# Kernel optimization log

Measured on AMD Instinct MI355X. Metric: run time of the kernel, lower is better.

Reference implementation:

```python
import jax, jax.numpy as jnp
import numpy as np

IN_DIM = 128
OUT_DIM = 128
EDGE_DIM = 64
NUM_HEADS = 8
HEAD_DIM = OUT_DIM // NUM_HEADS
N_NODES = 10000
N_EDGES = 320000
LN_EPS = 1e-5


def _gelu(x):
    # torch nn.GELU default is the exact (erf) formulation
    return jax.nn.gelu(x, approximate=False)


def _layernorm(x, g, b):
    mu = jnp.mean(x, axis=-1, keepdims=True)
    var = jnp.var(x, axis=-1, keepdims=True)
    return (x - mu) * jax.lax.rsqrt(var + LN_EPS) * g + b


def setup_inputs() -> dict:
    key = jax.random.key(0)
    ks = jax.random.split(key, 16)

    def lin(k, fan_in, fan_out):
        # torch nn.Linear default init: U(-1/sqrt(fan_in), 1/sqrt(fan_in))
        bound = 1.0 / np.sqrt(fan_in)
        kw, kb = jax.random.split(k)
        w = jax.random.uniform(kw, (fan_in, fan_out), jnp.float32, -bound, bound)
        b = jax.random.uniform(kb, (fan_out,), jnp.float32, -bound, bound)
        return w, b

    node_features = jax.random.normal(ks[0], (N_NODES, IN_DIM), jnp.float32)
    edge_index = jax.random.randint(ks[1], (2, N_EDGES), 0, N_NODES)
    edge_attr = jax.random.normal(ks[2], (N_EDGES, EDGE_DIM), jnp.float32)

    msg_w1, msg_b1 = lin(ks[3], 2 * IN_DIM + EDGE_DIM, OUT_DIM)
    msg_w2, msg_b2 = lin(ks[4], OUT_DIM, OUT_DIM)
    q_w, q_b = lin(ks[5], IN_DIM, OUT_DIM)
    kv_w, kv_b = lin(ks[6], IN_DIM + EDGE_DIM, OUT_DIM)
    out_w1, out_b1 = lin(ks[7], IN_DIM + OUT_DIM, OUT_DIM)
    out_w2, out_b2 = lin(ks[8], OUT_DIM, OUT_DIM)
    ln_g = 1.0 + 0.02 * jax.random.normal(ks[9], (OUT_DIM,), jnp.float32)
    ln_b = 0.02 * jax.random.normal(ks[10], (OUT_DIM,), jnp.float32)

    return dict(node_features=node_features, edge_attr=edge_attr,
                msg_w1=msg_w1, msg_b1=msg_b1, msg_w2=msg_w2, msg_b2=msg_b2,
                q_w=q_w, q_b=q_b, kv_w=kv_w, kv_b=kv_b,
                out_w1=out_w1, out_b1=out_b1, out_w2=out_w2, out_b2=out_b2,
                ln_g=ln_g, ln_b=ln_b, edge_index=edge_index)


def reference(node_features, edge_attr, msg_w1, msg_b1, msg_w2, msg_b2,
              q_w, q_b, kv_w, kv_b, out_w1, out_b1, out_w2, out_b2,
              ln_g, ln_b, edge_index):
    N = node_features.shape[0]
    E = edge_index.shape[1]
    src, dst = edge_index[0], edge_index[1]

    s = node_features[src]                      # [E, Din]
    d = node_features[dst]                      # [E, Din]

    # message MLP
    m_in = jnp.concatenate([s, d, edge_attr], axis=-1)          # [E, 2*Din+De]
    m = _gelu(m_in @ msg_w1 + msg_b1) @ msg_w2 + msg_b2         # [E, Dout]

    # per-edge attention logits
    q = (d @ q_w + q_b).reshape(E, NUM_HEADS, HEAD_DIM)
    kv_in = jnp.concatenate([s, edge_attr], axis=-1)
    kv = (kv_in @ kv_w + kv_b).reshape(E, NUM_HEADS, HEAD_DIM)
    attn = jnp.sum(q * kv, axis=-1) * (HEAD_DIM ** -0.5)        # [E, H]

    # Deterministic version: pick the edge with the largest index per dst node.
    last = jnp.full((N,), -1, dtype=jnp.int32).at[dst].max(
        jnp.arange(E, dtype=jnp.int32))                          # [N]
    attn_full = jnp.where(last[:, None] >= 0,
                          attn[jnp.maximum(last, 0)],
                          -jnp.inf)                              # [N, H]
    # softmax over the NODE axis (dim=0), exactly as the torch code does;
    # -inf rows contribute 0, so using N instead of dst.max()+1 is identical.
    attn_norm = jax.nn.softmax(attn_full, axis=0)[dst]           # [E, H]

    m = (m.reshape(E, NUM_HEADS, HEAD_DIM) * attn_norm[..., None]).reshape(E, OUT_DIM)

    # scatter-add aggregation
    agg = jax.ops.segment_sum(m, dst, num_segments=N)            # [N, Dout]

    h_in = jnp.concatenate([node_features, agg], axis=-1)        # [N, Din+Dout]
    h = _gelu(h_in @ out_w1 + out_b1) @ out_w2 + out_b2          # [N, Dout]

    # res_proj is Identity since in_dim == out_dim; dropout is eval-mode no-op
    return _layernorm(node_features + h, ln_g, ln_b)
```

## Files before the change

kernel.cpp:

```cpp
#include <hip/hip_runtime.h>
#include <hip/hip_bf16.h>

#define NN 10000
#define NE 320000

typedef __bf16 bf16x8 __attribute__((ext_vector_type(8)));
typedef float  f32x4  __attribute__((ext_vector_type(4)));

__device__ __forceinline__ float bf2f(ushort u){
  union { uint i; float f; } c; c.i = ((uint)u) << 16; return c.f;
}
__device__ __forceinline__ ushort f2bf(float f){
  union { float f; uint i; } c; c.f = f;
  uint x = c.i;
  return (ushort)((x + 0x7FFFu + ((x >> 16) & 1u)) >> 16);
}
__device__ __forceinline__ float gelu_erf(float x){
  return 0.5f * x * (1.0f + erff(x * 0.70710678118654752f));
}
__device__ __forceinline__ float gelu_tanh(float x){
  float y = 0.7978845608028654f * (x + 0.044715f * x * x * x);
  float e = __expf(2.f * y);
  float th = 1.f - 2.f / (e + 1.f);
  return 0.5f * x * (1.f + th);
}
__device__ __forceinline__ uint encf(float f){
  uint u = __float_as_uint(f);
  return (u & 0x80000000u) ? ~u : (u | 0x80000000u);
}
__device__ __forceinline__ float decf(uint u){
  return __uint_as_float((u & 0x80000000u) ? (u & 0x7FFFFFFFu) : ~u);
}
#define MFMA16(a,b,c) __builtin_amdgcn_mfma_f32_16x16x32_bf16((a),(b),(c),0,0,0)

__global__ void k_detect(const uint* __restrict__ w, int* __restrict__ flag){
  int t = threadIdx.x;
  uint cnt = 0;
  for (int i = t; i < 4096; i += 256){
    uint v = w[i * 63];
    uint e = (v >> 7) & 0xFF;
    if (e >= 100 && e <= 140) cnt++;
  }
  __shared__ uint red[256];
  red[t] = cnt; __syncthreads();
  for (int s = 128; s > 0; s >>= 1){
    if (t < s) red[t] += red[t + s];
    __syncthreads();
  }
  if (t == 0) *flag = (red[0] < 2048) ? 1 : 0;
}

__global__ void k_prep(
    const void* NF0, const void* w1, const void* w2, const void* qw, const void* kvw,
    const void* ow1, const void* ow2,
    const void* b1, const void* b2, const void* qb, const void* kvb,
    const void* ob1, const void* ob2, const void* lg, const void* lb,
    ushort* NFc, float* Gagg, int* last, int* cnt, uint* Menc, float* S,
    ushort* SB, ushort* KVW2,
    ushort* W1aT, ushort* W1bT, ushort* W1cT, ushort* W2T, ushort* QT, ushort* KVT,
    ushort* O1T, ushort* O2T, const int* flag)
{
  int f = *flag;
  int idx = blockIdx.x * 256 + threadIdx.x;
  if (idx < 320000){
    if (f){
      float4 v = ((const float4*)NF0)[idx];
      ushort4 o; o.x=f2bf(v.x); o.y=f2bf(v.y); o.z=f2bf(v.z); o.w=f2bf(v.w);
      ((ushort4*)NFc)[idx] = o;
    } else ((ushort4*)NFc)[idx] = ((const ushort4*)NF0)[idx];
    return;
  }
  idx -= 320000;
  if (idx < 320000){ float4 z = {0.f,0.f,0.f,0.f}; ((float4*)Gagg)[idx] = z; return; }
  idx -= 320000;
  if (idx < 20016){
    if (idx < 10000) last[idx] = -1;
    else if (idx < 20000) cnt[idx - 10000] = 0;
    else if (idx < 20008) Menc[idx - 20000] = 0u;
    else S[idx - 20008] = 0.f;
    return;
  }
  idx -= 20016;
  if (idx < 1024){
    const void* ps[8] = {b1,b2,qb,kvb,ob1,ob2,lg,lb};
    const void* p = ps[idx >> 7]; int j = idx & 127;
    SB[idx] = f ? f2bf(((const float*)p)[j]) : ((const ushort*)p)[j];
    return;
  }
  idx -= 1024;
  if (idx < 8192){
    KVW2[idx] = f ? f2bf(((const float*)kvw)[16384 + idx]) : ((const ushort*)kvw)[16384 + idx];
    return;
  }
  idx -= 8192;
  if (idx < 16384){ int c=idx>>7,k=idx&127; W1aT[idx] = f? f2bf(((const float*)w1)[k*128+c]) : ((const ushort*)w1)[k*128+c]; return; }
  idx -= 16384;
  if (idx < 16384){ int c=idx>>7,k=idx&127; W1bT[idx] = f? f2bf(((const float*)w1)[(128+k)*128+c]) : ((const ushort*)w1)[(128+k)*128+c]; return; }
  idx -= 16384;
  if (idx < 8192){ int c=idx>>6,k=idx&63;  W1cT[idx] = f? f2bf(((const float*)w1)[(256+k)*128+c]) : ((const ushort*)w1)[(256+k)*128+c]; return; }
  idx -= 8192;
  if (idx < 16384){ int c=idx>>7,k=idx&127; W2T[idx] = f? f2bf(((const float*)w2)[k*128+c]) : ((const ushort*)w2)[k*128+c]; return; }
  idx -= 16384;
  if (idx < 16384){ int c=idx>>7,k=idx&127; QT[idx]  = f? f2bf(((const float*)qw)[k*128+c]) : ((const ushort*)qw)[k*128+c]; return; }
  idx -= 16384;
  if (idx < 16384){ int c=idx>>7,k=idx&127; KVT[idx] = f? f2bf(((const float*)kvw)[k*128+c]) : ((const ushort*)kvw)[k*128+c]; return; }
  idx -= 16384;
  if (idx < 32768){ int c=idx>>8,k=idx&255; O1T[idx] = f? f2bf(((const float*)ow1)[k*128+c]) : ((const ushort*)ow1)[k*128+c]; return; }
  idx -= 32768;
  if (idx < 16384){ int c=idx>>7,k=idx&127; O2T[idx] = f? f2bf(((const float*)ow2)[k*128+c]) : ((const ushort*)ow2)[k*128+c]; return; }
}

__global__ void k_count(const int* __restrict__ dst, int* __restrict__ cnt,
                        int* __restrict__ last){
  int e = blockIdx.x * 256 + threadIdx.x;
  if (e < NE){
    int d = dst[e];
    atomicAdd(&cnt[d], 1);
    atomicMax(&last[d], e);
  }
}

__global__ __launch_bounds__(1024) void k_scan(const int* __restrict__ cnt,
                                               int* __restrict__ fill){
  __shared__ int sc[1024];
  int t = threadIdx.x;
  int base = t * 10;
  int v[10]; int tot = 0;
  #pragma unroll
  for (int j = 0; j < 10; ++j){
    int idx = base + j;
    v[j] = (idx < NN) ? cnt[idx] : 0;
    tot += v[j];
  }
  sc[t] = tot; __syncthreads();
  for (int off = 1; off < 1024; off <<= 1){
    int x = (t >= off) ? sc[t - off] : 0;
    __syncthreads();
    sc[t] += x;
    __syncthreads();
  }
  int run = sc[t] - tot;
  #pragma unroll
  for (int j = 0; j < 10; ++j){
    int idx = base + j;
    if (idx < NN) fill[idx] = run;
    run += v[j];
  }
}

__global__ void k_fill(const int* __restrict__ src, const int* __restrict__ dst,
                       int* __restrict__ fill, int* __restrict__ pos,
                       int* __restrict__ sSort, int* __restrict__ dSort){
  int e = blockIdx.x * 256 + threadIdx.x;
  if (e < NE){
    int d = dst[e];
    int p = atomicAdd(&fill[d], 1);
    pos[e] = p;
    sSort[p] = src[e];
    dSort[p] = d;
  }
}

__global__ __launch_bounds__(256) void k_perm(
    const float* __restrict__ EAf, const ushort* __restrict__ EAb,
    const int* __restrict__ pos, ushort* __restrict__ EAs,
    const int* __restrict__ flag)
{
  int i = blockIdx.x * 256 + threadIdx.x;
  int r = i >> 1, half = i & 1;
  if (r >= NE) return;
  int p = pos[r];
  ushort* op = EAs + (size_t)p * 64 + half * 32;
  if (*flag){
    const float* in = EAf + (size_t)r * 64 + half * 32;
    #pragma unroll
    for (int j = 0; j < 4; ++j){
      float4 a = *reinterpret_cast<const float4*>(in + j * 8);
      float4 b = *reinterpret_cast<const float4*>(in + j * 8 + 4);
      bf16x8 v;
      v[0]=(__bf16)a.x; v[1]=(__bf16)a.y; v[2]=(__bf16)a.z; v[3]=(__bf16)a.w;
      v[4]=(__bf16)b.x; v[5]=(__bf16)b.y; v[6]=(__bf16)b.z; v[7]=(__bf16)b.w;
      *reinterpret_cast<bf16x8*>(op + j * 8) = v;
    }
  } else {
    const ushort* in = EAb + (size_t)r * 64 + half * 32;
    #pragma unroll
    for (int j = 0; j < 4; ++j)
      *reinterpret_cast<bf16x8*>(op + j * 8) =
        *reinterpret_cast<const bf16x8*>(in + j * 8);
  }
}

__global__ __launch_bounds__(256) void k_nodepack(
    const ushort* __restrict__ NFc,
    const ushort* __restrict__ W1aT, const ushort* __restrict__ W1bT,
    const ushort* __restrict__ QT,  const ushort* __restrict__ KVT,
    const ushort* __restrict__ SB,
    ushort* __restrict__ PA, ushort* __restrict__ PB,
    ushort* __restrict__ Qb, ushort* __restrict__ KV1)
{
  int t = threadIdx.x, l = t & 63, w = t >> 6;
  int m = l & 15, g = l >> 4;
  int row0 = blockIdx.x * 16;
  const ushort* WT = (w==0) ? W1aT : (w==1) ? W1bT : (w==2) ? QT : KVT;
  ushort*       OUT= (w==0) ? PA   : (w==1) ? PB   : (w==2) ? Qb : KV1;
  const f32x4 FZ = {0.f,0.f,0.f,0.f};
  f32x4 acc[8];
  #pragma unroll
  for (int i = 0; i < 8; ++i) acc[i] = FZ;
  int arow = row0 + m;
  #pragma unroll
  for (int ks = 0; ks < 4; ++ks){
    int koff = ks * 32 + g * 8;
    bf16x8 a = *reinterpret_cast<const bf16x8*>(NFc + (size_t)arow * 128 + koff);
    #pragma unroll
    for (int nt = 0; nt < 8; ++nt){
      bf16x8 b = *reinterpret_cast<const bf16x8*>(WT + (size_t)(nt*16+m) * 128 + koff);
      acc[nt] = MFMA16(a, b, acc[nt]);
    }
  }
  #pragma unroll
  for (int nt = 0; nt < 8; ++nt){
    int col = nt * 16 + m;
    float bb = (w==1) ? bf2f(SB[col]) : (w==2) ? bf2f(SB[256+col]) : (w==3) ? bf2f(SB[384+col]) : 0.f;
    #pragma unroll
    for (int r = 0; r < 4; ++r){
      int row = row0 + g * 4 + r;
      OUT[(size_t)row * 128 + col] = f2bf(acc[nt][r] + bb);
    }
  }
}

__global__ __launch_bounds__(256) void k_edge(
    const ushort* __restrict__ PA, const ushort* __restrict__ PB,
    const ushort* __restrict__ EAs,
    const int* __restrict__ sSort, const int* __restrict__ dSort,
    const ushort* __restrict__ W1cT,
    float* __restrict__ Gagg)
{
  __shared__ int sIdx[128], dIdx[128];
  __shared__ __align__(16) char Hs[128 * 256];
  int t = threadIdx.x;
  int p0 = blockIdx.x * 128;
  int l = t & 63, w = t >> 6;
  int rw = w >> 1, cw = w & 1;
  int m = l & 15, g = l >> 4;

  if (t < 128){ sIdx[t] = sSort[p0 + t]; dIdx[t] = dSort[p0 + t]; }
  __syncthreads();

  {
    int r = t >> 1, half = t & 1;
    int sr = sIdx[r], dr = dIdx[r];
    #pragma unroll
    for (int j = 0; j < 8; ++j){
      int c8 = half * 8 + j;
      bf16x8 pa = *reinterpret_cast<const bf16x8*>(PA + (size_t)sr * 128 + c8 * 8);
      bf16x8 pb = *reinterpret_cast<const bf16x8*>(PB + (size_t)dr * 128 + c8 * 8);
      bf16x8 ps;
      #pragma unroll
      for (int k = 0; k < 8; ++k) ps[k] = (__bf16)((float)pa[k] + (float)pb[k]);
      int byte = (r * 256 + c8 * 16) ^ ((r & 7) << 4);
      *reinterpret_cast<bf16x8*>(&Hs[byte]) = ps;
    }
  }

  const f32x4 FZ = {0.f,0.f,0.f,0.f};
  f32x4 acc[4][4];
  #pragma unroll
  for (int i = 0; i < 4; ++i)
    #pragma unroll
    for (int j = 0; j < 4; ++j) acc[i][j] = FZ;

  #pragma unroll
  for (int ks = 0; ks < 2; ++ks){
    bf16x8 af[4], bfr[4];
    #pragma unroll
    for (int rt = 0; rt < 4; ++rt){
      int rl = rw * 64 + rt * 16 + m;
      af[rt] = *reinterpret_cast<const bf16x8*>(EAs + (size_t)(p0 + rl) * 64 + ks * 32 + g * 8);
    }
    #pragma unroll
    for (int ct = 0; ct < 4; ++ct){
      int col = cw * 64 + ct * 16 + m;
      bfr[ct] = *reinterpret_cast<const bf16x8*>(W1cT + (size_t)col * 64 + ks * 32 + g * 8);
    }
    #pragma unroll
    for (int rt = 0; rt < 4; ++rt)
      #pragma unroll
      for (int ct = 0; ct < 4; ++ct)
        acc[rt][ct] = MFMA16(af[rt], bfr[ct], acc[rt][ct]);
  }
  __syncthreads();

  #pragma unroll
  for (int ct = 0; ct < 4; ++ct){
    int col = cw * 64 + ct * 16 + m;
    #pragma unroll
    for (int rt = 0; rt < 4; ++rt)
      #pragma unroll
      for (int r = 0; r < 4; ++r){
        int row = rw * 64 + rt * 16 + g * 4 + r;
        int byte = (row * 256 + col * 2) ^ ((row & 7) << 4);
        float v = gelu_tanh(acc[rt][ct][r] + bf2f(*reinterpret_cast<const ushort*>(&Hs[byte])));
        *reinterpret_cast<ushort*>(&Hs[byte]) = f2bf(v);
      }
  }
  __syncthreads();

  int c = t & 127, hh = t >> 7;
  int rS = hh * 64, rE = rS + 64;
  float run = 0.f;
  int cur = dIdx[rS];
  for (int r = rS; r < rE; ++r){
    int d = dIdx[r];
    if (d != cur){
      unsafeAtomicAdd(&Gagg[(size_t)cur * 128 + c], run);
      run = 0.f; cur = d;
    }
    int byte = (r * 256 + c * 2) ^ ((r & 7) << 4);
    run += bf2f(*reinterpret_cast<const ushort*>(&Hs[byte]));
  }
  unsafeAtomicAdd(&Gagg[(size_t)cur * 128 + c], run);
}

template<int K, int MODE>
__global__ __launch_bounds__(256) void k_gemm(
    const ushort* __restrict__ A, const ushort* __restrict__ WT,
    const ushort* __restrict__ bias, void* __restrict__ out, int M)
{
  int t = threadIdx.x;
  int l = t & 63, w = t >> 6;
  int m = l & 15, g = l >> 4;
  int row0 = blockIdx.x * 64 + w * 16;
  const f32x4 FZ = {0.f,0.f,0.f,0.f};
  f32x4 acc[8];
  #pragma unroll
  for (int i = 0; i < 8; ++i) acc[i] = FZ;

  int arow = row0 + m; if (arow >= M) arow = M - 1;
  #pragma unroll
  for (int ks = 0; ks < K / 32; ++ks){
    int koff = ks * 32 + g * 8;
    bf16x8 a = *reinterpret_cast<const bf16x8*>(A + (size_t)arow * K + koff);
    #pragma unroll
    for (int nt = 0; nt < 8; ++nt){
      bf16x8 b = *reinterpret_cast<const bf16x8*>(WT + (size_t)(nt * 16 + m) * K + koff);
      acc[nt] = MFMA16(a, b, acc[nt]);
    }
  }
  #pragma unroll
  for (int nt = 0; nt < 8; ++nt){
    int col = nt * 16 + m;
    float bb = bf2f(bias[col]);
    #pragma unroll
    for (int r = 0; r < 4; ++r){
      int row = row0 + g * 4 + r;
      if (row < M){
        float v = acc[nt][r] + bb;
        if (MODE == 1) v = gelu_erf(v);
        ((ushort*)out)[(size_t)row * 128 + col] = f2bf(v);
      }
    }
  }
}

__global__ __launch_bounds__(256) void k_attn(
    const ushort* __restrict__ Qb, const ushort* __restrict__ KV1,
    const ushort* __restrict__ EAb, const float* __restrict__ EAf,
    const ushort* __restrict__ KVW2,
    const int* __restrict__ srcI, const int* __restrict__ last,
    float* __restrict__ attn, uint* __restrict__ Menc, const int* __restrict__ flag)
{
  __shared__ float ea_s[16][64];
  __shared__ int eN[16], sN[16];
  __shared__ uint lmax[8];
  int t = threadIdx.x;
  int n0 = blockIdx.x * 16;
  if (t < 16){
    int e = last[n0 + t];
    eN[t] = e;
    sN[t] = (e >= 0) ? srcI[e] : 0;
  }
  if (t < 8) lmax[t] = 0u;
  __syncthreads();
  int F = *flag;
  for (int i = t; i < 1024; i += 256){
    int nn = i >> 6, k = i & 63;
    int e = eN[nn];
    int ee = (e >= 0) ? e : 0;
    float v = F ? EAf[(size_t)ee * 64 + k] : bf2f(EAb[(size_t)ee * 64 + k]);
    ea_s[nn][k] = (e >= 0) ? v : 0.0f;
  }
  __syncthreads();

  int j = t & 127;
  int half = t >> 7;
  float acc[8];
  #pragma unroll
  for (int i = 0; i < 8; ++i) acc[i] = 0.f;
  for (int k = 0; k < 64; ++k){
    float wv = bf2f(KVW2[(size_t)k * 128 + j]);
    #pragma unroll
    for (int nn = 0; nn < 8; ++nn) acc[nn] += ea_s[half * 8 + nn][k] * wv;
  }
  #pragma unroll
  for (int nn = 0; nn < 8; ++nn){
    int nl = half * 8 + nn;
    int n = n0 + nl;
    int e = eN[nl];
    float kvv = acc[nn] + bf2f(KV1[(size_t)sN[nl] * 128 + j]);
    float qv  = bf2f(Qb[(size_t)n * 128 + j]);
    float p = qv * kvv;
    p += __shfl_xor(p, 1); p += __shfl_xor(p, 2);
    p += __shfl_xor(p, 4); p += __shfl_xor(p, 8);
    if ((j & 15) == 0 && e >= 0){
      float v = p * 0.25f;
      attn[(size_t)n * 8 + (j >> 4)] = v;
      atomicMax(&lmax[j >> 4], encf(v));
    }
  }
  __syncthreads();
  if (t < 8 && lmax[t]) atomicMax(&Menc[t], lmax[t]);
}

__global__ __launch_bounds__(256) void k_asum(
    const float* __restrict__ attn, const int* __restrict__ last,
    const uint* __restrict__ Menc, float* __restrict__ S)
{
  __shared__ float red[256][8];
  int t = threadIdx.x;
  float M[8];
  #pragma unroll
  for (int h = 0; h < 8; ++h) M[h] = decf(Menc[h]);
  float p[8];
  #pragma unroll
  for (int h = 0; h < 8; ++h) p[h] = 0.f;
  for (int n = blockIdx.x * 256 + t; n < NN; n += gridDim.x * 256){
    if (last[n] >= 0){
      #pragma unroll
      for (int h = 0; h < 8; ++h) p[h] += __expf(attn[(size_t)n * 8 + h] - M[h]);
    }
  }
  #pragma unroll
  for (int h = 0; h < 8; ++h) red[t][h] = p[h];
  __syncthreads();
  for (int s = 128; s > 0; s >>= 1){
    if (t < s){
      #pragma unroll
      for (int h = 0; h < 8; ++h) red[t][h] += red[t + s][h];
    }
    __syncthreads();
  }
  if (t < 8) atomicAdd(&S[t], red[0][t]);
}

__global__ __launch_bounds__(256) void k_aggmm(
    const float* __restrict__ Gagg, const ushort* __restrict__ W2T,
    const ushort* __restrict__ SB,
    const int* __restrict__ cnt, const int* __restrict__ last,
    const float* __restrict__ attn, const uint* __restrict__ Menc,
    const float* __restrict__ S,
    const ushort* __restrict__ NFc, ushort* __restrict__ h_in)
{
  int t = threadIdx.x, l = t & 63, w = t >> 6;
  int m = l & 15, g = l >> 4;
  int row0 = blockIdx.x * 64 + w * 16;

  {
    int rr = blockIdx.x * 64 + (t >> 2);
    int cc = (t & 3) * 32;
    if (rr < NN){
      #pragma unroll
      for (int j = 0; j < 4; ++j){
        bf16x8 v = *reinterpret_cast<const bf16x8*>(NFc + (size_t)rr * 128 + cc + j * 8);
        *reinterpret_cast<bf16x8*>(h_in + (size_t)rr * 256 + cc + j * 8) = v;
      }
    }
  }

  float M[8], Sinv[8];
  #pragma unroll
  for (int h = 0; h < 8; ++h){ M[h] = decf(Menc[h]); Sinv[h] = 1.0f / S[h]; }

  int arow = row0 + m; if (arow >= NN) arow = NN - 1;
  const f32x4 FZ = {0.f,0.f,0.f,0.f};
  f32x4 acc[8];
  #pragma unroll
  for (int i = 0; i < 8; ++i) acc[i] = FZ;

  #pragma unroll
  for (int ks = 0; ks < 4; ++ks){
    const float* gp = Gagg + (size_t)arow * 128 + ks * 32 + g * 8;
    float4 u0 = *reinterpret_cast<const float4*>(gp);
    float4 u1 = *reinterpret_cast<const float4*>(gp + 4);
    float gv[8] = {u0.x,u0.y,u0.z,u0.w,u1.x,u1.y,u1.z,u1.w};
    bf16x8 hi, lo;
    #pragma unroll
    for (int k = 0; k < 8; ++k){
      hi[k] = (__bf16)gv[k];
      lo[k] = (__bf16)(gv[k] - (float)hi[k]);
    }
    #pragma unroll
    for (int nt = 0; nt < 8; ++nt){
      bf16x8 b = *reinterpret_cast<const bf16x8*>(W2T + (size_t)(nt*16+m) * 128 + ks * 32 + g * 8);
      acc[nt] = MFMA16(hi, b, acc[nt]);
      acc[nt] = MFMA16(lo, b, acc[nt]);
    }
  }

  #pragma unroll
  for (int r = 0; r < 4; ++r){
    int row = row0 + g * 4 + r;
    if (row < NN){
      float cn = (float)cnt[row];
      int lst = last[row];
      #pragma unroll
      for (int nt = 0; nt < 8; ++nt){
        int col = nt * 16 + m;
        float bb = bf2f(SB[128 + col]);
        float aw = (lst >= 0) ? __expf(attn[(size_t)row * 8 + nt] - M[nt]) * Sinv[nt] : 0.f;
        float v = (acc[nt][r] + cn * bb) * aw;
        h_in[(size_t)row * 256 + 128 + col] = f2bf(v);
      }
    }
  }
}

__global__ __launch_bounds__(256) void k_out2ln(
    const ushort* __restrict__ T1, const ushort* __restrict__ O2T,
    const ushort* __restrict__ SB,
    const ushort* __restrict__ NFc, void* __restrict__ out,
    const int* __restrict__ flag)
{
  int t = threadIdx.x, l = t & 63, w = t >> 6;
  int m = l & 15, g = l >> 4;
  int row0 = blockIdx.x * 64 + w * 16;
  int F = *flag;
  int arow = row0 + m; if (arow >= NN) arow = NN - 1;
  const f32x4 FZ = {0.f,0.f,0.f,0.f};
  f32x4 acc[8];
  #pragma unroll
  for (int i = 0; i < 8; ++i) acc[i] = FZ;
  #pragma unroll
  for (int ks = 0; ks < 4; ++ks){
    int koff = ks * 32 + g * 8;
    bf16x8 a = *reinterpret_cast<const bf16x8*>(T1 + (size_t)arow * 128 + koff);
    #pragma unroll
    for (int nt = 0; nt < 8; ++nt){
      bf16x8 b = *reinterpret_cast<const bf16x8*>(O2T + (size_t)(nt*16+m) * 128 + koff);
      acc[nt] = MFMA16(a, b, acc[nt]);
    }
  }
  #pragma unroll
  for (int r = 0; r < 4; ++r){
    int row = row0 + g * 4 + r;
    bool ok = row < NN;
    int rr = ok ? row : NN - 1;
    float x[8]; float s = 0.f, q = 0.f;
    #pragma unroll
    for (int nt = 0; nt < 8; ++nt){
      int col = nt * 16 + m;
      float xv = acc[nt][r] + bf2f(SB[640 + col]) + bf2f(NFc[(size_t)rr * 128 + col]);
      x[nt] = xv; s += xv; q += xv * xv;
    }
    #pragma unroll
    for (int msk = 1; msk < 16; msk <<= 1){
      s += __shfl_xor(s, msk);
      q += __shfl_xor(q, msk);
    }
    float mean = s * (1.0f / 128.0f);
    float var  = q * (1.0f / 128.0f) - mean * mean;
    float rs = rsqrtf(var + 1e-5f);
    if (ok){
      #pragma unroll
      for (int nt = 0; nt < 8; ++nt){
        int col = nt * 16 + m;
        float y = (x[nt] - mean) * rs * bf2f(SB[768 + col]) + bf2f(SB[896 + col]);
        if (F) ((float*)out)[(size_t)row * 128 + col] = y;
        else   ((ushort*)out)[(size_t)row * 128 + col] = f2bf(y);
      }
    }
  }
}

extern "C" void kernel_launch(void* const* d_in, const int* in_sizes, int n_in,
                              void* d_out, int out_size, void* d_ws, size_t ws_size,
                              hipStream_t stream)
{
  const void* NF0  = d_in[0];
  const void* EA0  = d_in[1];
  const void* w1   = d_in[2];
  const void* b1   = d_in[3];
  const void* w2   = d_in[4];
  const void* b2   = d_in[5];
  const void* qw   = d_in[6];
  const void* qb   = d_in[7];
  const void* kvw  = d_in[8];
  const void* kvb  = d_in[9];
  const void* ow1  = d_in[10];
  const void* ob1  = d_in[11];
  const void* ow2  = d_in[12];
  const void* ob2  = d_in[13];
  const void* lg   = d_in[14];
  const void* lb   = d_in[15];
  const int*  srcI = (const int*)d_in[16];
  const int*  dstI = srcI + NE;

  char* ws = (char*)d_ws;
  size_t off = 0;
  auto alloc = [&](size_t bytes) -> void* {
    void* p = ws + off;
    off = (off + bytes + 255) & ~(size_t)255;
    return p;
  };
  int*    flag  = (int*)   alloc(4);
  ushort* NFc   = (ushort*)alloc((size_t)NN * 128 * 2);
  ushort* SB    = (ushort*)alloc(8 * 128 * 2);
  ushort* KVW2  = (ushort*)alloc(64 * 128 * 2);
  ushort* W1aT  = (ushort*)alloc(128 * 128 * 2);
  ushort* W1bT  = (ushort*)alloc(128 * 128 * 2);
  ushort* W1cT  = (ushort*)alloc(128 * 64 * 2);
  ushort* W2T   = (ushort*)alloc(128 * 128 * 2);
  ushort* QT    = (ushort*)alloc(128 * 128 * 2);
  ushort* KVT   = (ushort*)alloc(128 * 128 * 2);
  ushort* O1T   = (ushort*)alloc(128 * 256 * 2);
  ushort* O2T   = (ushort*)alloc(128 * 128 * 2);
  int*    last  = (int*)   alloc(NN * 4);
  int*    cnt   = (int*)   alloc(NN * 4);
  int*    fill  = (int*)   alloc(NN * 4);
  int*    pos   = (int*)   alloc((size_t)NE * 4);
  int*    sSort = (int*)   alloc((size_t)NE * 4);
  int*    dSort = (int*)   alloc((size_t)NE * 4);
  ushort* EAs   = (ushort*)alloc((size_t)NE * 64 * 2);
  float*  attn  = (float*) alloc(NN * 8 * 4);
  uint*   Menc  = (uint*)  alloc(8 * 4);
  float*  S     = (float*) alloc(8 * 4);
  ushort* PA    = (ushort*)alloc((size_t)NN * 128 * 2);
  ushort* PB    = (ushort*)alloc((size_t)NN * 128 * 2);
  ushort* Qb    = (ushort*)alloc((size_t)NN * 128 * 2);
  ushort* KV1   = (ushort*)alloc((size_t)NN * 128 * 2);
  float*  Gagg  = (float*) alloc((size_t)NN * 128 * 4);
  ushort* h_in  = (ushort*)alloc((size_t)NN * 256 * 2);
  ushort* T1    = (ushort*)alloc((size_t)NN * 128 * 2);

  k_detect<<<1, 256, 0, stream>>>((const uint*)NF0, flag);
  k_prep<<<3159, 256, 0, stream>>>(NF0, w1, w2, qw, kvw, ow1, ow2,
                                   b1, b2, qb, kvb, ob1, ob2, lg, lb,
                                   NFc, Gagg, last, cnt, Menc, S, SB, KVW2,
                                   W1aT, W1bT, W1cT, W2T, QT, KVT, O1T, O2T, flag);
  k_count<<<1250, 256, 0, stream>>>(dstI, cnt, last);
  k_scan<<<1, 1024, 0, stream>>>(cnt, fill);
  k_fill<<<1250, 256, 0, stream>>>(srcI, dstI, fill, pos, sSort, dSort);
  k_perm<<<2500, 256, 0, stream>>>((const float*)EA0, (const ushort*)EA0, pos, EAs, flag);
  k_nodepack<<<625, 256, 0, stream>>>(NFc, W1aT, W1bT, QT, KVT, SB, PA, PB, Qb, KV1);
  k_edge<<<2500, 256, 0, stream>>>(PA, PB, EAs, sSort, dSort, W1cT, Gagg);
  k_attn<<<625, 256, 0, stream>>>(Qb, KV1, (const ushort*)EA0, (const float*)EA0,
                                  KVW2, srcI, last, attn, Menc, flag);
  k_asum<<<40, 256, 0, stream>>>(attn, last, Menc, S);
  k_aggmm<<<157, 256, 0, stream>>>(Gagg, W2T, SB, cnt, last, attn, Menc, S, NFc, h_in);
  k_gemm<256, 1><<<157, 256, 0, stream>>>(h_in, O1T, SB + 512, T1, NN);
  k_out2ln<<<157, 256, 0, stream>>>(T1, O2T, SB, NFc, d_out, flag);
}
```

Before: 240.7 us.

## Fuse kernel launches: merge count into prep, fill+perm+nodepack, edge+attn, aggmm+gemm

Cuts the launch sequence by merging kernels. Edge counting moves into the prep kernel, and init gets its own small kernel. Fill, edge-attr permutation and node projections share one launch, using shared memory to hold positions so the pos buffer is gone. Edge MLP and attention logits share one launch, and the PA+PB gather is moved into the segmented reduction. The aggregation GEMM and out_w1 GEMM are fused through LDS, so the h_in buffer is no longer written. This saves launch overhead and global round-trips, at the cost of heterogeneous blocks within a launch and more register and LDS pressure.

```diff
diff --git a/kernel.cpp b/kernel.cpp
--- a/kernel.cpp
+++ b/kernel.cpp
@@ -33,35 +33,53 @@
 }
 #define MFMA16(a,b,c) __builtin_amdgcn_mfma_f32_16x16x32_bf16((a),(b),(c),0,0,0)
 
-__global__ void k_detect(const uint* __restrict__ w, int* __restrict__ flag){
+__global__ void k_init(const uint* __restrict__ w, int* __restrict__ flag,
+                       int* __restrict__ cnt, int* __restrict__ last,
+                       uint* __restrict__ Menc, float* __restrict__ S){
   int t = threadIdx.x;
-  uint cnt = 0;
-  for (int i = t; i < 4096; i += 256){
-    uint v = w[i * 63];
-    uint e = (v >> 7) & 0xFF;
-    if (e >= 100 && e <= 140) cnt++;
-  }
-  __shared__ uint red[256];
-  red[t] = cnt; __syncthreads();
-  for (int s = 128; s > 0; s >>= 1){
-    if (t < s) red[t] += red[t + s];
-    __syncthreads();
-  }
-  if (t == 0) *flag = (red[0] < 2048) ? 1 : 0;
+  if (blockIdx.x == 0){
+    uint c = 0;
+    for (int i = t; i < 4096; i += 256){
+      uint v = w[i * 63];
+      uint e = (v >> 7) & 0xFF;
+      if (e >= 100 && e <= 140) c++;
+    }
+    __shared__ uint red[256];
+    red[t] = c; __syncthreads();
+    for (int s = 128; s > 0; s >>= 1){
+      if (t < s) red[t] += red[t + s];
+      __syncthreads();
+    }
+    if (t == 0) *flag = (red[0] < 2048) ? 1 : 0;
+    return;
+  }
+  int idx = (blockIdx.x - 1) * 256 + t;
+  if (idx < 10000) last[idx] = -1;
+  else if (idx < 20000) cnt[idx - 10000] = 0;
+  else if (idx < 20008) Menc[idx - 20000] = 0u;
+  else if (idx < 20016) S[idx - 20008] = 0.f;
 }
 
 __global__ void k_prep(
-    const void* NF0, const void* w1, const void* w2, const void* qw, const void* kvw,
+    const void* NF0, const int* __restrict__ dstI,
+    const void* w1, const void* w2, const void* qw, const void* kvw,
     const void* ow1, const void* ow2,
     const void* b1, const void* b2, const void* qb, const void* kvb,
     const void* ob1, const void* ob2, const void* lg, const void* lb,
-    ushort* NFc, float* Gagg, int* last, int* cnt, uint* Menc, float* S,
-    ushort* SB, ushort* KVW2,
+    int* __restrict__ cnt, int* __restrict__ last,
+    ushort* NFc, float* Gagg, ushort* SB, ushort* KVW2,
     ushort* W1aT, ushort* W1bT, ushort* W1cT, ushort* W2T, ushort* QT, ushort* KVT,
-    ushort* O1T, ushort* O2T, const int* flag)
+    ushort* O1aT, ushort* O1bT, ushort* O2T, const int* flag)
 {
   int f = *flag;
   int idx = blockIdx.x * 256 + threadIdx.x;
+  if (idx < NE){
+    int d = dstI[idx];
+    atomicAdd(&cnt[d], 1);
+    atomicMax(&last[d], idx);
+    return;
+  }
+  idx -= NE;
   if (idx < 320000){
     if (f){
       float4 v = ((const float4*)NF0)[idx];
@@ -73,14 +91,6 @@
   idx -= 320000;
   if (idx < 320000){ float4 z = {0.f,0.f,0.f,0.f}; ((float4*)Gagg)[idx] = z; return; }
   idx -= 320000;
-  if (idx < 20016){
-    if (idx < 10000) last[idx] = -1;
-    else if (idx < 20000) cnt[idx - 10000] = 0;
-    else if (idx < 20008) Menc[idx - 20000] = 0u;
-    else S[idx - 20008] = 0.f;
-    return;
-  }
-  idx -= 20016;
   if (idx < 1024){
     const void* ps[8] = {b1,b2,qb,kvb,ob1,ob2,lg,lb};
     const void* p = ps[idx >> 7]; int j = idx & 127;
@@ -105,19 +115,11 @@
   idx -= 16384;
   if (idx < 16384){ int c=idx>>7,k=idx&127; KVT[idx] = f? f2bf(((const float*)kvw)[k*128+c]) : ((const ushort*)kvw)[k*128+c]; return; }
   idx -= 16384;
-  if (idx < 32768){ int c=idx>>8,k=idx&255; O1T[idx] = f? f2bf(((const float*)ow1)[k*128+c]) : ((const ushort*)ow1)[k*128+c]; return; }
-  idx -= 32768;
+  if (idx < 16384){ int c=idx>>7,k=idx&127; O1aT[idx] = f? f2bf(((const float*)ow1)[k*128+c]) : ((const ushort*)ow1)[k*128+c]; return; }
+  idx -= 16384;
+  if (idx < 16384){ int c=idx>>7,k=idx&127; O1bT[idx] = f? f2bf(((const float*)ow1)[(128+k)*128+c]) : ((const ushort*)ow1)[(128+k)*128+c]; return; }
+  idx -= 16384;
   if (idx < 16384){ int c=idx>>7,k=idx&127; O2T[idx] = f? f2bf(((const float*)ow2)[k*128+c]) : ((const ushort*)ow2)[k*128+c]; return; }
-}
-
-__global__ void k_count(const int* __restrict__ dst, int* __restrict__ cnt,
-                        int* __restrict__ last){
-  int e = blockIdx.x * 256 + threadIdx.x;
-  if (e < NE){
-    int d = dst[e];
-    atomicAdd(&cnt[d], 1);
-    atomicMax(&last[d], e);
-  }
 }
 
 __global__ __launch_bounds__(1024) void k_scan(const int* __restrict__ cnt,
@@ -148,280 +150,232 @@
   }
 }
 
-__global__ void k_fill(const int* __restrict__ src, const int* __restrict__ dst,
-                       int* __restrict__ fill, int* __restrict__ pos,
-                       int* __restrict__ sSort, int* __restrict__ dSort){
-  int e = blockIdx.x * 256 + threadIdx.x;
-  if (e < NE){
-    int d = dst[e];
-    int p = atomicAdd(&fill[d], 1);
-    pos[e] = p;
-    sSort[p] = src[e];
-    dSort[p] = d;
-  }
-}
-
-__global__ __launch_bounds__(256) void k_perm(
+__global__ __launch_bounds__(256) void k_fillperm(
+    const int* __restrict__ srcI, const int* __restrict__ dstI,
+    int* __restrict__ fill, int* __restrict__ sSort, int* __restrict__ dSort,
     const float* __restrict__ EAf, const ushort* __restrict__ EAb,
-    const int* __restrict__ pos, ushort* __restrict__ EAs,
-    const int* __restrict__ flag)
-{
-  int i = blockIdx.x * 256 + threadIdx.x;
-  int r = i >> 1, half = i & 1;
-  if (r >= NE) return;
-  int p = pos[r];
-  ushort* op = EAs + (size_t)p * 64 + half * 32;
-  if (*flag){
-    const float* in = EAf + (size_t)r * 64 + half * 32;
-    #pragma unroll
-    for (int j = 0; j < 4; ++j){
-      float4 a = *reinterpret_cast<const float4*>(in + j * 8);
-      float4 b = *reinterpret_cast<const float4*>(in + j * 8 + 4);
-      bf16x8 v;
-      v[0]=(__bf16)a.x; v[1]=(__bf16)a.y; v[2]=(__bf16)a.z; v[3]=(__bf16)a.w;
-      v[4]=(__bf16)b.x; v[5]=(__bf16)b.y; v[6]=(__bf16)b.z; v[7]=(__bf16)b.w;
-      *reinterpret_cast<bf16x8*>(op + j * 8) = v;
-    }
-  } else {
-    const ushort* in = EAb + (size_t)r * 64 + half * 32;
-    #pragma unroll
-    for (int j = 0; j < 4; ++j)
-      *reinterpret_cast<bf16x8*>(op + j * 8) =
-        *reinterpret_cast<const bf16x8*>(in + j * 8);
-  }
-}
-
-__global__ __launch_bounds__(256) void k_nodepack(
+    ushort* __restrict__ EAs,
     const ushort* __restrict__ NFc,
     const ushort* __restrict__ W1aT, const ushort* __restrict__ W1bT,
     const ushort* __restrict__ QT,  const ushort* __restrict__ KVT,
     const ushort* __restrict__ SB,
     ushort* __restrict__ PA, ushort* __restrict__ PB,
-    ushort* __restrict__ Qb, ushort* __restrict__ KV1)
+    ushort* __restrict__ Qb, ushort* __restrict__ KV1,
+    const int* __restrict__ flag)
 {
-  int t = threadIdx.x, l = t & 63, w = t >> 6;
-  int m = l & 15, g = l >> 4;
-  int row0 = blockIdx.x * 16;
-  const ushort* WT = (w==0) ? W1aT : (w==1) ? W1bT : (w==2) ? QT : KVT;
-  ushort*       OUT= (w==0) ? PA   : (w==1) ? PB   : (w==2) ? Qb : KV1;
-  const f32x4 FZ = {0.f,0.f,0.f,0.f};
-  f32x4 acc[8];
-  #pragma unroll
-  for (int i = 0; i < 8; ++i) acc[i] = FZ;
-  int arow = row0 + m;
-  #pragma unroll
-  for (int ks = 0; ks < 4; ++ks){
-    int koff = ks * 32 + g * 8;
-    bf16x8 a = *reinterpret_cast<const bf16x8*>(NFc + (size_t)arow * 128 + koff);
+  int t = threadIdx.x;
+  if (blockIdx.x >= 1250){
+    int l = t & 63, w = t >> 6;
+    int m = l & 15, g = l >> 4;
+    int row0 = ((int)blockIdx.x - 1250) * 16;
+    const ushort* WT = (w==0) ? W1aT : (w==1) ? W1bT : (w==2) ? QT : KVT;
+    ushort*       OUT= (w==0) ? PA   : (w==1) ? PB   : (w==2) ? Qb : KV1;
+    const f32x4 FZ = {0.f,0.f,0.f,0.f};
+    f32x4 acc[8];
+    #pragma unroll
+    for (int i = 0; i < 8; ++i) acc[i] = FZ;
+    int arow = row0 + m;
+    #pragma unroll
+    for (int ks = 0; ks < 4; ++ks){
+      int koff = ks * 32 + g * 8;
+      bf16x8 a = *reinterpret_cast<const bf16x8*>(NFc + (size_t)arow * 128 + koff);
+      #pragma unroll
+      for (int nt = 0; nt < 8; ++nt){
+        bf16x8 b = *reinterpret_cast<const bf16x8*>(WT + (size_t)(nt*16+m) * 128 + koff);
+        acc[nt] = MFMA16(a, b, acc[nt]);
+      }
+    }
     #pragma unroll
     for (int nt = 0; nt < 8; ++nt){
-      bf16x8 b = *reinterpret_cast<const bf16x8*>(WT + (size_t)(nt*16+m) * 128 + koff);
-      acc[nt] = MFMA16(a, b, acc[nt]);
-    }
-  }
-  #pragma unroll
-  for (int nt = 0; nt < 8; ++nt){
-    int col = nt * 16 + m;
-    float bb = (w==1) ? bf2f(SB[col]) : (w==2) ? bf2f(SB[256+col]) : (w==3) ? bf2f(SB[384+col]) : 0.f;
-    #pragma unroll
-    for (int r = 0; r < 4; ++r){
-      int row = row0 + g * 4 + r;
-      OUT[(size_t)row * 128 + col] = f2bf(acc[nt][r] + bb);
-    }
-  }
-}
-
-__global__ __launch_bounds__(256) void k_edge(
+      int col = nt * 16 + m;
+      float bb = (w==1) ? bf2f(SB[col]) : (w==2) ? bf2f(SB[256+col]) : (w==3) ? bf2f(SB[384+col]) : 0.f;
+      #pragma unroll
+      for (int r = 0; r < 4; ++r){
+        int row = row0 + g * 4 + r;
+        OUT[(size_t)row * 128 + col] = f2bf(acc[nt][r] + bb);
+      }
+    }
+    return;
+  }
+  __shared__ int sp[256];
+  int e0 = blockIdx.x * 256;
+  int e = e0 + t;
+  {
+    int d = dstI[e];
+    int p = atomicAdd(&fill[d], 1);
+    sSort[p] = srcI[e];
+    dSort[p] = d;
+    sp[t] = p;
+  }
+  __syncthreads();
+  if (*flag){
+    #pragma unroll
+    for (int pass = 0; pass < 16; ++pass){
+      int i = pass * 256 + t;
+      int rloc = i >> 4, q = i & 15;
+      int p = sp[rloc];
+      float4 v = *reinterpret_cast<const float4*>(EAf + (size_t)(e0 + rloc) * 64 + q * 4);
+      ushort4 o; o.x=f2bf(v.x); o.y=f2bf(v.y); o.z=f2bf(v.z); o.w=f2bf(v.w);
+      *reinterpret_cast<ushort4*>(EAs + (size_t)p * 64 + q * 4) = o;
+    }
+  } else {
+    #pragma unroll
+    for (int pass = 0; pass < 8; ++pass){
+      int i = pass * 256 + t;
+      int rloc = i >> 3, q = i & 7;
+      int p = sp[rloc];
+      *reinterpret_cast<bf16x8*>(EAs + (size_t)p * 64 + q * 8) =
+        *reinterpret_cast<const bf16x8*>(EAb + (size_t)(e0 + rloc) * 64 + q * 8);
+    }
+  }
+}
+
+__global__ __launch_bounds__(256) void k_edgeattn(
     const ushort* __restrict__ PA, const ushort* __restrict__ PB,
     const ushort* __restrict__ EAs,
     const int* __restrict__ sSort, const int* __restrict__ dSort,
     const ushort* __restrict__ W1cT,
-    float* __restrict__ Gagg)
-{
-  __shared__ int sIdx[128], dIdx[128];
-  __shared__ __align__(16) char Hs[128 * 256];
-  int t = threadIdx.x;
-  int p0 = blockIdx.x * 128;
-  int l = t & 63, w = t >> 6;
-  int rw = w >> 1, cw = w & 1;
-  int m = l & 15, g = l >> 4;
-
-  if (t < 128){ sIdx[t] = sSort[p0 + t]; dIdx[t] = dSort[p0 + t]; }
-  __syncthreads();
-
-  {
-    int r = t >> 1, half = t & 1;
-    int sr = sIdx[r], dr = dIdx[r];
-    #pragma unroll
-    for (int j = 0; j < 8; ++j){
-      int c8 = half * 8 + j;
-      bf16x8 pa = *reinterpret_cast<const bf16x8*>(PA + (size_t)sr * 128 + c8 * 8);
-      bf16x8 pb = *reinterpret_cast<const bf16x8*>(PB + (size_t)dr * 128 + c8 * 8);
-      bf16x8 ps;
-      #pragma unroll
-      for (int k = 0; k < 8; ++k) ps[k] = (__bf16)((float)pa[k] + (float)pb[k]);
-      int byte = (r * 256 + c8 * 16) ^ ((r & 7) << 4);
-      *reinterpret_cast<bf16x8*>(&Hs[byte]) = ps;
-    }
-  }
-
-  const f32x4 FZ = {0.f,0.f,0.f,0.f};
-  f32x4 acc[4][4];
-  #pragma unroll
-  for (int i = 0; i < 4; ++i)
-    #pragma unroll
-    for (int j = 0; j < 4; ++j) acc[i][j] = FZ;
-
-  #pragma unroll
-  for (int ks = 0; ks < 2; ++ks){
-    bf16x8 af[4], bfr[4];
-    #pragma unroll
-    for (int rt = 0; rt < 4; ++rt){
-      int rl = rw * 64 + rt * 16 + m;
-      af[rt] = *reinterpret_cast<const bf16x8*>(EAs + (size_t)(p0 + rl) * 64 + ks * 32 + g * 8);
-    }
-    #pragma unroll
-    for (int ct = 0; ct < 4; ++ct){
-      int col = cw * 64 + ct * 16 + m;
-      bfr[ct] = *reinterpret_cast<const bf16x8*>(W1cT + (size_t)col * 64 + ks * 32 + g * 8);
-    }
-    #pragma unroll
-    for (int rt = 0; rt < 4; ++rt)
-      #pragma unroll
-      for (int ct = 0; ct < 4; ++ct)
-        acc[rt][ct] = MFMA16(af[rt], bfr[ct], acc[rt][ct]);
-  }
-  __syncthreads();
-
-  #pragma unroll
-  for (int ct = 0; ct < 4; ++ct){
-    int col = cw * 64 + ct * 16 + m;
-    #pragma unroll
-    for (int rt = 0; rt < 4; ++rt)
-      #pragma unroll
-      for (int r = 0; r < 4; ++r){
-        int row = rw * 64 + rt * 16 + g * 4 + r;
-        int byte = (row * 256 + col * 2) ^ ((row & 7) << 4);
-        float v = gelu_tanh(acc[rt][ct][r] + bf2f(*reinterpret_cast<const ushort*>(&Hs[byte])));
-        *reinterpret_cast<ushort*>(&Hs[byte]) = f2bf(v);
-      }
-  }
-  __syncthreads();
-
-  int c = t & 127, hh = t >> 7;
-  int rS = hh * 64, rE = rS + 64;
-  float run = 0.f;
-  int cur = dIdx[rS];
-  for (int r = rS; r < rE; ++r){
-    int d = dIdx[r];
-    if (d != cur){
-      unsafeAtomicAdd(&Gagg[(size_t)cur * 128 + c], run);
-      run = 0.f; cur = d;
-    }
-    int byte = (r * 256 + c * 2) ^ ((r & 7) << 4);
-    run += bf2f(*reinterpret_cast<const ushort*>(&Hs[byte]));
-  }
-  unsafeAtomicAdd(&Gagg[(size_t)cur * 128 + c], run);
-}
-
-template<int K, int MODE>
-__global__ __launch_bounds__(256) void k_gemm(
-    const ushort* __restrict__ A, const ushort* __restrict__ WT,
-    const ushort* __restrict__ bias, void* __restrict__ out, int M)
-{
-  int t = threadIdx.x;
-  int l = t & 63, w = t >> 6;
-  int m = l & 15, g = l >> 4;
-  int row0 = blockIdx.x * 64 + w * 16;
-  const f32x4 FZ = {0.f,0.f,0.f,0.f};
-  f32x4 acc[8];
-  #pragma unroll
-  for (int i = 0; i < 8; ++i) acc[i] = FZ;
-
-  int arow = row0 + m; if (arow >= M) arow = M - 1;
-  #pragma unroll
-  for (int ks = 0; ks < K / 32; ++ks){
-    int koff = ks * 32 + g * 8;
-    bf16x8 a = *reinterpret_cast<const bf16x8*>(A + (size_t)arow * K + koff);
-    #pragma unroll
-    for (int nt = 0; nt < 8; ++nt){
-      bf16x8 b = *reinterpret_cast<const bf16x8*>(WT + (size_t)(nt * 16 + m) * K + koff);
-      acc[nt] = MFMA16(a, b, acc[nt]);
-    }
-  }
-  #pragma unroll
-  for (int nt = 0; nt < 8; ++nt){
-    int col = nt * 16 + m;
-    float bb = bf2f(bias[col]);
-    #pragma unroll
-    for (int r = 0; r < 4; ++r){
-      int row = row0 + g * 4 + r;
-      if (row < M){
-        float v = acc[nt][r] + bb;
-        if (MODE == 1) v = gelu_erf(v);
-        ((ushort*)out)[(size_t)row * 128 + col] = f2bf(v);
-      }
-    }
-  }
-}
-
-__global__ __launch_bounds__(256) void k_attn(
+    float* __restrict__ Gagg,
     const ushort* __restrict__ Qb, const ushort* __restrict__ KV1,
     const ushort* __restrict__ EAb, const float* __restrict__ EAf,
     const ushort* __restrict__ KVW2,
     const int* __restrict__ srcI, const int* __restrict__ last,
     float* __restrict__ attn, uint* __restrict__ Menc, const int* __restrict__ flag)
 {
+  __shared__ int sIdx[128], dIdx[128];
+  __shared__ __align__(16) char Hs[128 * 256];
   __shared__ float ea_s[16][64];
   __shared__ int eN[16], sN[16];
   __shared__ uint lmax[8];
   int t = threadIdx.x;
-  int n0 = blockIdx.x * 16;
-  if (t < 16){
-    int e = last[n0 + t];
-    eN[t] = e;
-    sN[t] = (e >= 0) ? srcI[e] : 0;
-  }
-  if (t < 8) lmax[t] = 0u;
+
+  if (blockIdx.x >= 2500){
+    int n0 = ((int)blockIdx.x - 2500) * 16;
+    if (t < 16){
+      int e = last[n0 + t];
+      eN[t] = e;
+      sN[t] = (e >= 0) ? srcI[e] : 0;
+    }
+    if (t < 8) lmax[t] = 0u;
+    __syncthreads();
+    int F = *flag;
+    for (int i = t; i < 1024; i += 256){
+      int nn = i >> 6, k = i & 63;
+      int e = eN[nn];
+      int ee = (e >= 0) ? e : 0;
+      float v = F ? EAf[(size_t)ee * 64 + k] : bf2f(EAb[(size_t)ee * 64 + k]);
+      ea_s[nn][k] = (e >= 0) ? v : 0.0f;
+    }
+    __syncthreads();
+    int j = t & 127;
+    int half = t >> 7;
+    float acc[8];
+    #pragma unroll
+    for (int i = 0; i < 8; ++i) acc[i] = 0.f;
+    for (int k = 0; k < 64; ++k){
+      float wv = bf2f(KVW2[(size_t)k * 128 + j]);
+      #pragma unroll
+      for (int nn = 0; nn < 8; ++nn) acc[nn] += ea_s[half * 8 + nn][k] * wv;
+    }
+    #pragma unroll
+    for (int nn = 0; nn < 8; ++nn){
+      int nl = half * 8 + nn;
+      int n = n0 + nl;
+      int e = eN[nl];
+      float kvv = acc[nn] + bf2f(KV1[(size_t)sN[nl] * 128 + j]);
+      float qv  = bf2f(Qb[(size_t)n * 128 + j]);
+      float p = qv * kvv;
+      p += __shfl_xor(p, 1); p += __shfl_xor(p, 2);
+      p += __shfl_xor(p, 4); p += __shfl_xor(p, 8);
+      if ((j & 15) == 0 && e >= 0){
+        float v = p * 0.25f;
+        attn[(size_t)n * 8 + (j >> 4)] = v;
+        atomicMax(&lmax[j >> 4], encf(v));
+      }
+    }
+    __syncthreads();
+    if (t < 8 && lmax[t]) atomicMax(&Menc[t], lmax[t]);
+    return;
+  }
+
+  int p0 = blockIdx.x * 128;
+  int l = t & 63, w = t >> 6;
+  int rw = w >> 1, cw = w & 1;
+  int m = l & 15, g = l >> 4;
+
+  if (t < 128){ sIdx[t] = sSort[p0 + t]; dIdx[t] = dSort[p0 + t]; }
+
+  const f32x4 FZ = {0.f,0.f,0.f,0.f};
+  f32x4 acc[4][4];
+  #pragma unroll
+  for (int i = 0; i < 4; ++i)
+    #pragma unroll
+    for (int j = 0; j < 4; ++j) acc[i][j] = FZ;
+
+  #pragma unroll
+  for (int ks = 0; ks < 2; ++ks){
+    bf16x8 af[4], bfr[4];
+    #pragma unroll
+    for (int rt = 0; rt < 4; ++rt){
+      int rl = rw * 64 + rt * 16 + m;
+      af[rt] = *reinterpret_cast<const bf16x8*>(EAs + (size_t)(p0 + rl) * 64 + ks * 32 + g * 8);
+    }
+    #pragma unroll
+    for (int ct = 0; ct < 4; ++ct){
+      int col = cw * 64 + ct * 16 + m;
+      bfr[ct] = *reinterpret_cast<const bf16x8*>(W1cT + (size_t)col * 64 + ks * 32 + g * 8);
+    }
+    #pragma unroll
+    for (int rt = 0; rt < 4; ++rt)
+      #pragma unroll
+      for (int ct = 0; ct < 4; ++ct)
+        acc[rt][ct] = MFMA16(af[rt], bfr[ct], acc[rt][ct]);
+  }
+
+  #pragma unroll
+  for (int ct = 0; ct < 4; ++ct){
+    int col = cw * 64 + ct * 16 + m;
+    #pragma unroll
+    for (int rt = 0; rt < 4; ++rt)
+      #pragma unroll
+      for (int r = 0; r < 4; ++r){
+        int row = rw * 64 + rt * 16 + g * 4 + r;
+        int byte = (row * 256 + col * 2) ^ ((row & 7) << 4);
+        *reinterpret_cast<ushort*>(&Hs[byte]) = f2bf(acc[rt][ct][r]);
+      }
+  }
   __syncthreads();
-  int F = *flag;
-  for (int i = t; i < 1024; i += 256){
-    int nn = i >> 6, k = i & 63;
-    int e = eN[nn];
-    int ee = (e >= 0) ? e : 0;
-    float v = F ? EAf[(size_t)ee * 64 + k] : bf2f(EAb[(size_t)ee * 64 + k]);
-    ea_s[nn][k] = (e >= 0) ? v : 0.0f;
-  }
-  __syncthreads();
-
-  int j = t & 127;
-  int half = t >> 7;
-  float acc[8];
-  #pragma unroll
-  for (int i = 0; i < 8; ++i) acc[i] = 0.f;
-  for (int k = 0; k < 64; ++k){
-    float wv = bf2f(KVW2[(size_t)k * 128 + j]);
-    #pragma unroll
-    for (int nn = 0; nn < 8; ++nn) acc[nn] += ea_s[half * 8 + nn][k] * wv;
-  }
-  #pragma unroll
-  for (int nn = 0; nn < 8; ++nn){
-    int nl = half * 8 + nn;
-    int n = n0 + nl;
-    int e = eN[nl];
-    float kvv = acc[nn] + bf2f(KV1[(size_t)sN[nl] * 128 + j]);
-    float qv  = bf2f(Qb[(size_t)n * 128 + j]);
-    float p = qv * kvv;
-    p += __shfl_xor(p, 1); p += __shfl_xor(p, 2);
-    p += __shfl_xor(p, 4); p += __shfl_xor(p, 8);
-    if ((j & 15) == 0 && e >= 0){
-      float v = p * 0.25f;
-      attn[(size_t)n * 8 + (j >> 4)] = v;
-      atomicMax(&lmax[j >> 4], encf(v));
-    }
-  }
-  __syncthreads();
-  if (t < 8 && lmax[t]) atomicMax(&Menc[t], lmax[t]);
+
+  {
+    int o = t & 15, rg = t >> 4;
+    int base = rg * 8;
+    float s8[8];
+    #pragma unroll
+    for (int k = 0; k < 8; ++k) s8[k] = 0.f;
+    int cur = dIdx[base];
+    #pragma unroll
+    for (int j = 0; j < 8; ++j){
+      int row = base + j;
+      int d = dIdx[row], sr = sIdx[row];
+      if (d != cur){
+        #pragma unroll
+        for (int k = 0; k < 8; ++k)
+          unsafeAtomicAdd(&Gagg[(size_t)cur * 128 + o * 8 + k], s8[k]);
+        #pragma unroll
+        for (int k = 0; k < 8; ++k) s8[k] = 0.f;
+        cur = d;
+      }
+      bf16x8 a8 = *reinterpret_cast<const bf16x8*>(&Hs[row * 256 + ((o ^ j) << 4)]);
+      bf16x8 pa = *reinterpret_cast<const bf16x8*>(PA + (size_t)sr * 128 + o * 8);
+      bf16x8 pb = *reinterpret_cast<const bf16x8*>(PB + (size_t)d  * 128 + o * 8);
+      #pragma unroll
+      for (int k = 0; k < 8; ++k)
+        s8[k] += gelu_tanh((float)a8[k] + (float)pa[k] + (float)pb[k]);
+    }
+    #pragma unroll
+    for (int k = 0; k < 8; ++k)
+      unsafeAtomicAdd(&Gagg[(size_t)cur * 128 + o * 8 + k], s8[k]);
+  }
 }
 
 __global__ __launch_bounds__(256) void k_asum(
@@ -455,29 +409,19 @@
   if (t < 8) atomicAdd(&S[t], red[0][t]);
 }
 
-__global__ __launch_bounds__(256) void k_aggmm(
+__global__ __launch_bounds__(256) void k_aggmm2(
     const float* __restrict__ Gagg, const ushort* __restrict__ W2T,
+    const ushort* __restrict__ O1aT, const ushort* __restrict__ O1bT,
     const ushort* __restrict__ SB,
     const int* __restrict__ cnt, const int* __restrict__ last,
     const float* __restrict__ attn, const uint* __restrict__ Menc,
     const float* __restrict__ S,
-    const ushort* __restrict__ NFc, ushort* __restrict__ h_in)
+    const ushort* __restrict__ NFc, ushort* __restrict__ T1)
 {
+  __shared__ __align__(16) char Zs[64 * 256];
   int t = threadIdx.x, l = t & 63, w = t >> 6;
   int m = l & 15, g = l >> 4;
   int row0 = blockIdx.x * 64 + w * 16;
-
-  {
-    int rr = blockIdx.x * 64 + (t >> 2);
-    int cc = (t & 3) * 32;
-    if (rr < NN){
-      #pragma unroll
-      for (int j = 0; j < 4; ++j){
-        bf16x8 v = *reinterpret_cast<const bf16x8*>(NFc + (size_t)rr * 128 + cc + j * 8);
-        *reinterpret_cast<bf16x8*>(h_in + (size_t)rr * 256 + cc + j * 8) = v;
-      }
-    }
-  }
 
   float M[8], Sinv[8];
   #pragma unroll
@@ -512,16 +456,48 @@
   #pragma unroll
   for (int r = 0; r < 4; ++r){
     int row = row0 + g * 4 + r;
-    if (row < NN){
-      float cn = (float)cnt[row];
-      int lst = last[row];
-      #pragma unroll
-      for (int nt = 0; nt < 8; ++nt){
-        int col = nt * 16 + m;
-        float bb = bf2f(SB[128 + col]);
-        float aw = (lst >= 0) ? __expf(attn[(size_t)row * 8 + nt] - M[nt]) * Sinv[nt] : 0.f;
-        float v = (acc[nt][r] + cn * bb) * aw;
-        h_in[(size_t)row * 256 + 128 + col] = f2bf(v);
+    int rr = (row < NN) ? row : NN - 1;
+    float cn = (float)cnt[rr];
+    int lst = last[rr];
+    int Lr = w * 16 + g * 4 + r;
+    #pragma unroll
+    for (int nt = 0; nt < 8; ++nt){
+      int col = nt * 16 + m;
+      float aw = (lst >= 0) ? __expf(attn[(size_t)rr * 8 + nt] - M[nt]) * Sinv[nt] : 0.f;
+      float z = (acc[nt][r] + cn * bf2f(SB[128 + col])) * aw;
+      int byte = (Lr * 256 + col * 2) ^ ((Lr & 7) << 4);
+      *reinterpret_cast<ushort*>(&Zs[byte]) = f2bf(z);
+    }
+  }
+  __syncthreads();
+
+  f32x4 acc2[8];
+  #pragma unroll
+  for (int i = 0; i < 8; ++i) acc2[i] = FZ;
+  int La = w * 16 + m;
+  #pragma unroll
+  for (int ks = 0; ks < 4; ++ks){
+    int koff = ks * 32 + g * 8;
+    bf16x8 az = *reinterpret_cast<const bf16x8*>(&Zs[(La * 256 + koff * 2) ^ ((La & 7) << 4)]);
+    bf16x8 an = *reinterpret_cast<const bf16x8*>(NFc + (size_t)arow * 128 + koff);
+    #pragma unroll
+    for (int nt = 0; nt < 8; ++nt){
+      bf16x8 b1v = *reinterpret_cast<const bf16x8*>(O1bT + (size_t)(nt*16+m) * 128 + koff);
+      bf16x8 b2v = *reinterpret_cast<const bf16x8*>(O1aT + (size_t)(nt*16+m) * 128 + koff);
+      acc2[nt] = MFMA16(az, b1v, acc2[nt]);
+      acc2[nt] = MFMA16(an, b2v, acc2[nt]);
+    }
+  }
+  #pragma unroll
+  for (int nt = 0; nt < 8; ++nt){
+    int col = nt * 16 + m;
+    float bb = bf2f(SB[512 + col]);
+    #pragma unroll
+    for (int r = 0; r < 4; ++r){
+      int row = row0 + g * 4 + r;
+      if (row < NN){
+        float v = gelu_erf(acc2[nt][r] + bb);
+        T1[(size_t)row * 128 + col] = f2bf(v);
       }
     }
   }
@@ -624,12 +600,12 @@
   ushort* W2T   = (ushort*)alloc(128 * 128 * 2);
   ushort* QT    = (ushort*)alloc(128 * 128 * 2);
   ushort* KVT   = (ushort*)alloc(128 * 128 * 2);
-  ushort* O1T   = (ushort*)alloc(128 * 256 * 2);
+  ushort* O1aT  = (ushort*)alloc(128 * 128 * 2);
+  ushort* O1bT  = (ushort*)alloc(128 * 128 * 2);
   ushort* O2T   = (ushort*)alloc(128 * 128 * 2);
   int*    last  = (int*)   alloc(NN * 4);
   int*    cnt   = (int*)   alloc(NN * 4);
   int*    fill  = (int*)   alloc(NN * 4);
-  int*    pos   = (int*)   alloc((size_t)NE * 4);
   int*    sSort = (int*)   alloc((size_t)NE * 4);
   int*    dSort = (int*)   alloc((size_t)NE * 4);
   ushort* EAs   = (ushort*)alloc((size_t)NE * 64 * 2);
@@ -641,24 +617,23 @@
   ushort* Qb    = (ushort*)alloc((size_t)NN * 128 * 2);
   ushort* KV1   = (ushort*)alloc((size_t)NN * 128 * 2);
   float*  Gagg  = (float*) alloc((size_t)NN * 128 * 4);
-  ushort* h_in  = (ushort*)alloc((size_t)NN * 256 * 2);
   ushort* T1    = (ushort*)alloc((size_t)NN * 128 * 2);
 
-  k_detect<<<1, 256, 0, stream>>>((const uint*)NF0, flag);
-  k_prep<<<3159, 256, 0, stream>>>(NF0, w1, w2, qw, kvw, ow1, ow2,
+  k_init<<<80, 256, 0, stream>>>((const uint*)NF0, flag, cnt, last, Menc, S);
+  k_prep<<<4330, 256, 0, stream>>>(NF0, dstI, w1, w2, qw, kvw, ow1, ow2,
                                    b1, b2, qb, kvb, ob1, ob2, lg, lb,
-                                   NFc, Gagg, last, cnt, Menc, S, SB, KVW2,
-                                   W1aT, W1bT, W1cT, W2T, QT, KVT, O1T, O2T, flag);
-  k_count<<<1250, 256, 0, stream>>>(dstI, cnt, last);
+                                   cnt, last, NFc, Gagg, SB, KVW2,
+                                   W1aT, W1bT, W1cT, W2T, QT, KVT, O1aT, O1bT, O2T, flag);
   k_scan<<<1, 1024, 0, stream>>>(cnt, fill);
-  k_fill<<<1250, 256, 0, stream>>>(srcI, dstI, fill, pos, sSort, dSort);
-  k_perm<<<2500, 256, 0, stream>>>((const float*)EA0, (const ushort*)EA0, pos, EAs, flag);
-  k_nodepack<<<625, 256, 0, stream>>>(NFc, W1aT, W1bT, QT, KVT, SB, PA, PB, Qb, KV1);
-  k_edge<<<2500, 256, 0, stream>>>(PA, PB, EAs, sSort, dSort, W1cT, Gagg);
-  k_attn<<<625, 256, 0, stream>>>(Qb, KV1, (const ushort*)EA0, (const float*)EA0,
-                                  KVW2, srcI, last, attn, Menc, flag);
+  k_fillperm<<<1875, 256, 0, stream>>>(srcI, dstI, fill, sSort, dSort,
+                                       (const float*)EA0, (const ushort*)EA0, EAs,
+                                       NFc, W1aT, W1bT, QT, KVT, SB,
+                                       PA, PB, Qb, KV1, flag);
+  k_edgeattn<<<3125, 256, 0, stream>>>(PA, PB, EAs, sSort, dSort, W1cT, Gagg,
+                                       Qb, KV1, (const ushort*)EA0, (const float*)EA0,
+                                       KVW2, srcI, last, attn, Menc, flag);
   k_asum<<<40, 256, 0, stream>>>(attn, last, Menc, S);
-  k_aggmm<<<157, 256, 0, stream>>>(Gagg, W2T, SB, cnt, last, attn, Menc, S, NFc, h_in);
-  k_gemm<256, 1><<<157, 256, 0, stream>>>(h_in, O1T, SB + 512, T1, NN);
+  k_aggmm2<<<157, 256, 0, stream>>>(Gagg, W2T, O1aT, O1bT, SB, cnt, last,
+                                    attn, Menc, S, NFc, T1);
   k_out2ln<<<157, 256, 0, stream>>>(T1, O2T, SB, NFc, d_out, flag);
 }
```

New measurement: 355.8 us. 47.8% more time.
